# Kernel tuning notes

Hardware: AMD Instinct MI355X
Metric: run time of the kernel (lower is better)

## Reference

```python
import jax, jax.numpy as jnp
import numpy as np

H = 256
W = 256
RADIUS = 1.5
TAU = 1.0
EPS = 1e-8


def _ndc_grid(h, w):
    ys, xs = jnp.meshgrid(jnp.arange(h, dtype=jnp.float32), jnp.arange(w, dtype=jnp.float32), indexing='ij')
    xs = xs / (w - 1) * 2.0 - 1.0
    ys = ys / (h - 1) * 2.0 - 1.0
    return jnp.stack([xs.ravel(), ys.ravel()], 0)  # [2, N]


def _make_rt(key, b, v):
    # near-identity extrinsics: identity rotation + small random translation
    t = jax.random.normal(key, (b, v, 3), dtype=jnp.float32) * 0.05
    rt = jnp.tile(jnp.eye(4, dtype=jnp.float32), (b, v, 1, 1))
    rt = rt.at[:, :, :3, 3].set(t)
    return rt


def setup_inputs() -> dict:
    key = jax.random.key(0)
    ks = jax.random.split(key, 4)
    B, V, C = 2, 3, 32
    depths = jax.random.uniform(ks[0], (B, V, 1, H, W), jnp.float32, 1.0, 3.0)
    feats = jax.random.normal(ks[1], (B, V, C, H, W), jnp.float32)
    K = jnp.tile(jnp.eye(4, dtype=jnp.float32), (B, 1, 1))
    K = K.at[:, 0, 0].set(1.2).at[:, 1, 1].set(1.2)  # NDC-space focal lengths
    src_RTs = _make_rt(ks[2], B, V)
    src_RTinvs = jnp.linalg.inv(src_RTs)
    dst_RTs = _make_rt(ks[3], B, 1)
    dst_RTinvs = jnp.linalg.inv(dst_RTs)
    return {"depths": depths, "feats": feats, "K": K, "src_RTs": src_RTs,
            "src_RTinvs": src_RTinvs, "dst_RTs": dst_RTs, "dst_RTinvs": dst_RTinvs}


def _view_to_world(depth, K_inv, RTinv):
    # depth: [BV, 1, N] -> world homogeneous coords [BV, 4, N]
    grid = _ndc_grid(H, W)                                      # [2, N]
    xy = grid[None] * depth                                     # [BV, 2, N]
    pc = jnp.concatenate([xy, depth, jnp.ones_like(depth)], 1)  # [BV, 4, N]
    cam = jnp.einsum('bij,bjn->bin', K_inv, pc)
    return jnp.einsum('bij,bjn->bin', RTinv, cam)


def _world_to_view(wrld, K, RT):
    cam = jnp.einsum('bij,bjn->bin', RT, wrld)
    proj = jnp.einsum('bij,bjn->bin', K, cam)
    z = proj[:, 2:3]
    xy = proj[:, 0:2] / (z + EPS)
    xy = jnp.where(z <= 0.0, -10.0, xy)       # invalid points pushed off-screen
    return jnp.concatenate([xy, z], 1)        # [BV, 3, N]


def _splatter(pc, feats, radius):
    # pc: [BV, N, 3] (x_ndc, y_ndc, depth); feats: [BV, C, N]
    BV, N, _ = pc.shape
    C = feats.shape[1]
    x, y, z = pc[..., 0], pc[..., 1], pc[..., 2]
    px = (x + 1.0) * 0.5 * (W - 1)
    py = (y + 1.0) * 0.5 * (H - 1)
    offs = jnp.array([[dy, dx] for dy in (-1, 0, 1) for dx in (-1, 0, 1)], dtype=jnp.float32)
    ix = jnp.round(px)[..., None] + offs[:, 1]     # [BV, N, 9]
    iy = jnp.round(py)[..., None] + offs[:, 0]
    dist = jnp.sqrt((ix - px[..., None]) ** 2 + (iy - py[..., None]) ** 2 + EPS)
    w_r = jnp.maximum(0.0, 1.0 - dist / radius)    # radius-based falloff
    valid = (ix >= 0) & (ix < W) & (iy >= 0) & (iy < H) & (z[..., None] > 0)
    w_d = jnp.exp(-TAU * z)[..., None]             # depth-aware (soft z-buffer) weight
    w = w_r * w_d * valid.astype(w_r.dtype)        # [BV, N, 9]
    idx = iy.astype(jnp.int32).clip(0, H - 1) * W + ix.astype(jnp.int32).clip(0, W - 1)
    flat = (jnp.arange(BV, dtype=jnp.int32)[:, None, None] * (H * W) + idx).reshape(-1)
    w_sum = jax.ops.segment_sum(w.reshape(-1), flat, num_segments=BV * H * W)
    fw = (feats[:, :, :, None] * w[:, None, :, :]).transpose(0, 2, 3, 1).reshape(-1, C)
    f_sum = jax.ops.segment_sum(fw, flat, num_segments=BV * H * W)
    z_sum = jax.ops.segment_sum((z[..., None] * w).reshape(-1), flat, num_segments=BV * H * W)
    out_f = (f_sum / (w_sum[:, None] + EPS)).reshape(BV, H, W, C).transpose(0, 3, 1, 2)
    out_d = (z_sum / (w_sum + EPS)).reshape(BV, 1, H, W)
    return out_f, out_d


def reference(depths, feats, K, src_RTs, src_RTinvs, dst_RTs, dst_RTinvs):
    B, V, C = feats.shape[0], feats.shape[1], feats.shape[2]
    N = H * W
    d = depths.reshape(B * V, 1, N)
    f = feats.reshape(B * V, C, N)
    K_bv = jnp.repeat(K, V, axis=0)
    K_inv_bv = jnp.repeat(jnp.linalg.inv(K), V, axis=0)
    src_rtinv = src_RTinvs.reshape(B * V, 4, 4)
    dst_rt = jnp.repeat(dst_RTs[:, 0], V, axis=0)
    wrld = _view_to_world(d, K_inv_bv, src_rtinv)      # view -> world per source view
    sampler = _world_to_view(wrld, K_bv, dst_rt)       # world -> target view [BV,3,N]
    pc = sampler.transpose(0, 2, 1)                    # [BV, N, 3]
    prj_f, prj_d = _splatter(pc, f, RADIUS)
    return prj_f.reshape(B, V, C, H, W), prj_d.reshape(B, V, 1, H, W)
```

## Files before the change

kernel.cpp:

```cpp
#include <hip/hip_runtime.h>
#include <hip/hip_fp16.h>
#include <math.h>

#define H 256
#define W 256
#define HW (H * W)
#define B 2
#define V 3
#define BV (B * V)
#define C 32
#define RADIUS 1.5f
#define TAU 1.0f
#define EPS 1e-8f

#define NPIX (BV * HW)
#define NBLK (NPIX / 256)

#define GW 258
#define GH 258
#define NCELL (BV * GH * GW)
#define NSUMS ((NCELL + 255) / 256)
#define ECAP 384

__device__ __forceinline__ int swizzle_block(int bid) {
    return (bid & 7) * (NBLK / 8) + (bid >> 3);
}

__global__ void setup_kernel(const float* __restrict__ Kmat,
                             const float* __restrict__ srcRTinv,
                             const float* __restrict__ dstRT,
                             float* __restrict__ Mbuf) {
    int bv = threadIdx.x;
    if (bv >= BV) return;
    int b = bv / V;

    float a[4][8];
    for (int i = 0; i < 4; i++)
        for (int j = 0; j < 4; j++) {
            a[i][j] = Kmat[b * 16 + i * 4 + j];
            a[i][4 + j] = (i == j) ? 1.0f : 0.0f;
        }
    for (int col = 0; col < 4; col++) {
        int piv = col;
        float best = fabsf(a[col][col]);
        for (int r = col + 1; r < 4; r++) {
            float v = fabsf(a[r][col]);
            if (v > best) { best = v; piv = r; }
        }
        if (piv != col) {
            for (int j = 0; j < 8; j++) {
                float t = a[col][j]; a[col][j] = a[piv][j]; a[piv][j] = t;
            }
        }
        float s = 1.0f / a[col][col];
        for (int j = 0; j < 8; j++) a[col][j] *= s;
        for (int r = 0; r < 4; r++) {
            if (r == col) continue;
            float m = a[r][col];
            for (int j = 0; j < 8; j++) a[r][j] -= m * a[col][j];
        }
    }
    float Kinv[16];
    for (int i = 0; i < 4; i++)
        for (int j = 0; j < 4; j++) Kinv[i * 4 + j] = a[i][4 + j];

    float T1[16];
    const float* S = srcRTinv + bv * 16;
    for (int i = 0; i < 4; i++)
        for (int j = 0; j < 4; j++) {
            float acc = 0.0f;
            for (int k = 0; k < 4; k++) acc += S[i * 4 + k] * Kinv[k * 4 + j];
            T1[i * 4 + j] = acc;
        }
    float T2[16];
    const float* D = dstRT + b * 16;
    for (int i = 0; i < 4; i++)
        for (int j = 0; j < 4; j++) {
            float acc = 0.0f;
            for (int k = 0; k < 4; k++) acc += D[i * 4 + k] * T1[k * 4 + j];
            T2[i * 4 + j] = acc;
        }
    const float* Kb = Kmat + b * 16;
    for (int i = 0; i < 4; i++)
        for (int j = 0; j < 4; j++) {
            float acc = 0.0f;
            for (int k = 0; k < 4; k++) acc += Kb[i * 4 + k] * T2[k * 4 + j];
            Mbuf[bv * 16 + i * 4 + j] = acc;
        }
}

__global__ __launch_bounds__(256) void project_count_kernel(
    const float* __restrict__ depths, const float* __restrict__ Mbuf,
    float4* __restrict__ staging, int2* __restrict__ meta) {
    int gid = swizzle_block(blockIdx.x) * 256 + threadIdx.x;
    int bv = gid >> 16;
    int n = gid & (HW - 1);

    float xn = (float)(n & (W - 1)) * (2.0f / (W - 1)) - 1.0f;
    float yn = (float)(n >> 8)      * (2.0f / (H - 1)) - 1.0f;
    float d = depths[gid];
    const float* M = Mbuf + bv * 16;
    float X = xn * d, Y = yn * d;
    float p0 = M[0] * X + M[1] * Y + M[2] * d + M[3];
    float p1 = M[4] * X + M[5] * Y + M[6] * d + M[7];
    float z  = M[8] * X + M[9] * Y + M[10] * d + M[11];

    int cell = -1;
    float px = 0.0f, py = 0.0f;
    if (z > 0.0f) {
        float inv = 1.0f / (z + EPS);
        px = (p0 * inv + 1.0f) * 0.5f * (float)(W - 1);
        py = (p1 * inv + 1.0f) * 0.5f * (float)(H - 1);
        float rx = rintf(px), ry = rintf(py);
        if (rx >= -1.0f && rx <= (float)W && ry >= -1.0f && ry <= (float)H) {
            cell = bv * (GH * GW) + ((int)ry + 1) * GW + ((int)rx + 1);
            atomicAdd(&meta[cell].y, 1);
        }
    }
    staging[gid] = make_float4(px, py, z, __int_as_float(cell));
}

__global__ __launch_bounds__(256) void alloc1_kernel(int2* __restrict__ meta,
                                                     int* __restrict__ bsum) {
    int i = blockIdx.x * 256 + threadIdx.x;
    int c = (i < NCELL) ? meta[i].y : 0;
    int lane = threadIdx.x & 63;
    int wid = threadIdx.x >> 6;
    int x = c;
#pragma unroll
    for (int dlt = 1; dlt < 64; dlt <<= 1) {
        int y = __shfl_up(x, dlt);
        if (lane >= dlt) x += y;
    }
    __shared__ int wsum[4];
    __shared__ int wbase[4];
    if (lane == 63) wsum[wid] = x;
    __syncthreads();
    if (threadIdx.x == 0) {
        int s0 = wsum[0], s1 = wsum[1], s2 = wsum[2], s3 = wsum[3];
        wbase[0] = 0; wbase[1] = s0; wbase[2] = s0 + s1; wbase[3] = s0 + s1 + s2;
        bsum[blockIdx.x] = s0 + s1 + s2 + s3;
    }
    __syncthreads();
    if (i <= NCELL) meta[i].x = wbase[wid] + (x - c);
}

__global__ __launch_bounds__(256) void alloc2_kernel(int* __restrict__ bsum) {
    __shared__ int wsum[4];
    __shared__ int wbase[4];
    __shared__ int carry_s;
    int tid = threadIdx.x;
    int lane = tid & 63;
    int wid = tid >> 6;
    if (tid == 0) carry_s = 0;
    __syncthreads();
    const int nchunk = (NSUMS + 255) / 256;
    for (int ch = 0; ch < nchunk; ch++) {
        int i = ch * 256 + tid;
        int c = (i < NSUMS) ? bsum[i] : 0;
        int x = c;
#pragma unroll
        for (int dlt = 1; dlt < 64; dlt <<= 1) {
            int y = __shfl_up(x, dlt);
            if (lane >= dlt) x += y;
        }
        if (lane == 63) wsum[wid] = x;
        __syncthreads();
        if (tid == 0) {
            int cr = carry_s;
            int s0 = wsum[0], s1 = wsum[1], s2 = wsum[2], s3 = wsum[3];
            wbase[0] = cr; wbase[1] = cr + s0; wbase[2] = cr + s0 + s1;
            wbase[3] = cr + s0 + s1 + s2;
            carry_s = cr + s0 + s1 + s2 + s3;
        }
        __syncthreads();
        if (i < NSUMS) bsum[i] = wbase[wid] + (x - c);
        __syncthreads();
    }
}

__global__ __launch_bounds__(256) void fill_kernel(
    const float* __restrict__ feats, const float4* __restrict__ staging,
    const int* __restrict__ bsum, int2* __restrict__ meta,
    float4* __restrict__ entries16, uint4* __restrict__ entriesF) {
    __shared__ float sm[C][257];
    int blk = blockIdx.x;
    int bv = blk >> 8;
    int n0 = (blk & 255) << 8;
    int tid = threadIdx.x;
    const float* src = feats + (size_t)bv * C * HW + n0;
#pragma unroll
    for (int c = 0; c < C; c++) sm[c][tid] = src[(size_t)c * HW + tid];
    __syncthreads();

    int gid = (bv << 16) | (n0 + tid);
    float4 s = staging[gid];
    int cell = __float_as_int(s.w);
    if (cell < 0) return;
    int pos = bsum[cell >> 8] + atomicAdd(&meta[cell].x, 1);

    float wd = expf(-TAU * s.z);
    entries16[pos] = make_float4(s.x, s.y, s.z, wd);

    uint4* dst = entriesF + (size_t)pos * 4;
#pragma unroll
    for (int g = 0; g < 4; g++) {
        __half2 h0 = __floats2half2_rn(sm[g * 8 + 0][tid], sm[g * 8 + 1][tid]);
        __half2 h1 = __floats2half2_rn(sm[g * 8 + 2][tid], sm[g * 8 + 3][tid]);
        __half2 h2 = __floats2half2_rn(sm[g * 8 + 4][tid], sm[g * 8 + 5][tid]);
        __half2 h3 = __floats2half2_rn(sm[g * 8 + 6][tid], sm[g * 8 + 7][tid]);
        uint4 pk;
        pk.x = *(unsigned int*)&h0;
        pk.y = *(unsigned int*)&h1;
        pk.z = *(unsigned int*)&h2;
        pk.w = *(unsigned int*)&h3;
        dst[g] = pk;
    }
}

__global__ __launch_bounds__(256) void gather_kernel(
    const float4* __restrict__ entries16, const uint4* __restrict__ entriesF,
    const int2* __restrict__ meta, const int* __restrict__ bsum,
    float* __restrict__ out) {
    __shared__ int cs_s[18][19];
    __shared__ int row_rs[18];
    __shared__ int row_off[18];
    __shared__ int row_sl[18];
    __shared__ float4 lds_e[ECAP];
    __shared__ uint4 lds_f[ECAP * 5];

    int sblk = swizzle_block(blockIdx.x);
    int bv = sblk >> 8;
    int t = sblk & 255;
    int ty0 = (t >> 4) << 4;
    int tx0 = (t & 15) << 4;
    int tid = threadIdx.x;
    int cellbase = bv * (GH * GW);

    for (int i = tid; i < 18 * 19; i += 256) {
        int hr = i / 19, lc = i - hr * 19;
        int cg = cellbase + (ty0 + hr) * GW + (tx0 + lc);
        int2 m = meta[cg];
        cs_s[hr][lc] = bsum[cg >> 8] + m.x - m.y;
    }
    __syncthreads();
    if (tid == 0) {
        int off = 0;
        for (int hr = 0; hr < 18; hr++) {
            int rs = cs_s[hr][0];
            int len = cs_s[hr][18] - rs;
            int sl = min(len, ECAP - off);
            if (sl < 0) sl = 0;
            row_rs[hr] = rs;
            row_off[hr] = off;
            row_sl[hr] = sl;
            off += sl;
        }
    }
    __syncthreads();
    {
        int wid = tid >> 6, lane = tid & 63;
        for (int hr = wid; hr < 18; hr += 4) {
            int rs = row_rs[hr], off = row_off[hr], sl = row_sl[hr];
            for (int j = lane; j < sl; j += 64)
                lds_e[off + j] = entries16[rs + j];
            int j0 = lane >> 2, g = lane & 3;
            for (int j = j0; j < sl; j += 16)
                lds_f[(off + j) * 5 + g] = entriesF[(size_t)(rs + j) * 4 + g];
        }
    }
    __syncthreads();

    int lx = tid & 15, ly = tid >> 4;
    float qx = (float)(tx0 + lx);
    float qy = (float)(ty0 + ly);

    float wsum = 0.0f, zwsum = 0.0f;
    float facc[C];
#pragma unroll
    for (int c = 0; c < C; c++) facc[c] = 0.0f;

    auto accum_lds = [&](float4 v, int li) {
        float ddx = qx - v.x, ddy = qy - v.y;
        float d2 = ddx * ddx + ddy * ddy + EPS;
        if (d2 < RADIUS * RADIUS) {
            float dist = sqrtf(d2);
            float wr = 1.0f - dist * (1.0f / RADIUS);
            float w = wr * v.w;
            wsum += w;
            zwsum += v.z * w;
#pragma unroll
            for (int g = 0; g < 4; g++) {
                uint4 fv = lds_f[li * 5 + g];
                const __half2* h2 = (const __half2*)&fv;
#pragma unroll
                for (int k = 0; k < 4; k++) {
                    float2 f2 = __half22float2(h2[k]);
                    facc[g * 8 + 2 * k]     = fmaf(w, f2.x, facc[g * 8 + 2 * k]);
                    facc[g * 8 + 2 * k + 1] = fmaf(w, f2.y, facc[g * 8 + 2 * k + 1]);
                }
            }
        }
    };
    auto accum_glb = [&](float4 v, int pos) {
        float ddx = qx - v.x, ddy = qy - v.y;
        float d2 = ddx * ddx + ddy * ddy + EPS;
        if (d2 < RADIUS * RADIUS) {
            float dist = sqrtf(d2);
            float wr = 1.0f - dist * (1.0f / RADIUS);
            float w = wr * v.w;
            wsum += w;
            zwsum += v.z * w;
            const uint4* fp = entriesF + (size_t)pos * 4;
#pragma unroll
            for (int g = 0; g < 4; g++) {
                uint4 fv = fp[g];
                const __half2* h2 = (const __half2*)&fv;
#pragma unroll
                for (int k = 0; k < 4; k++) {
                    float2 f2 = __half22float2(h2[k]);
                    facc[g * 8 + 2 * k]     = fmaf(w, f2.x, facc[g * 8 + 2 * k]);
                    facc[g * 8 + 2 * k + 1] = fmaf(w, f2.y, facc[g * 8 + 2 * k + 1]);
                }
            }
        }
    };

#pragma unroll
    for (int dy = 0; dy < 3; dy++) {
        int hr = ly + dy;
        int s = cs_s[hr][lx];
        int e = cs_s[hr][lx + 3];
        int rs = row_rs[hr];
        int off = row_off[hr];
        int sEnd = rs + row_sl[hr];
        int e1 = min(e, sEnd);
        for (int pos = s; pos < e1; ++pos) {
            int li = off + (pos - rs);
            accum_lds(lds_e[li], li);
        }
        for (int pos = max(s, sEnd); pos < e; ++pos)
            accum_glb(entries16[pos], pos);
    }

    int q = ((ty0 + ly) << 8) | (tx0 + lx);
    int gid = (bv << 16) | q;
    float invw = 1.0f / (wsum + EPS);
    float* ob = out + (size_t)bv * C * HW + q;
#pragma unroll
    for (int c = 0; c < C; c++) ob[(size_t)c * HW] = facc[c] * invw;
    out[(size_t)BV * C * HW + gid] = zwsum * invw;
}

extern "C" void kernel_launch(void* const* d_in, const int* in_sizes, int n_in,
                              void* d_out, int out_size, void* d_ws, size_t ws_size,
                              hipStream_t stream) {
    const float* depths   = (const float*)d_in[0];
    const float* feats    = (const float*)d_in[1];
    const float* Kmat     = (const float*)d_in[2];
    const float* srcRTinv = (const float*)d_in[4];
    const float* dstRT    = (const float*)d_in[5];
    float* out = (float*)d_out;

    char* ws = (char*)d_ws;
    size_t off_entriesF = 0;
    size_t off_entries16 = off_entriesF + (size_t)NPIX * 64;
    size_t off_staging = off_entries16 + (size_t)NPIX * 16;
    size_t off_meta = off_staging + (size_t)NPIX * 16;
    size_t off_bsum = off_meta + (size_t)(NCELL + 1) * 8;
    size_t off_M = off_bsum + (size_t)NSUMS * 4 + 16;
    size_t needed = off_M + (size_t)BV * 16 * 4;

    if (ws_size < needed) {
        hipMemsetAsync(d_out, 0, (size_t)out_size * 4, stream);
        return;
    }

    uint4* entriesF   = (uint4*)(ws + off_entriesF);
    float4* entries16 = (float4*)(ws + off_entries16);
    float4* staging   = (float4*)(ws + off_staging);
    int2* meta        = (int2*)(ws + off_meta);
    int* bsum         = (int*)(ws + off_bsum);
    float* Mbuf       = (float*)(ws + off_M);

    hipMemsetAsync(meta, 0, (size_t)(NCELL + 1) * 8, stream);
    setup_kernel<<<1, 64, 0, stream>>>(Kmat, srcRTinv, dstRT, Mbuf);
    project_count_kernel<<<NBLK, 256, 0, stream>>>(depths, Mbuf, staging, meta);
    alloc1_kernel<<<NSUMS, 256, 0, stream>>>(meta, bsum);
    alloc2_kernel<<<1, 256, 0, stream>>>(bsum);
    fill_kernel<<<NBLK, 256, 0, stream>>>(feats, staging, bsum, meta,
                                          entries16, entriesF);
    gather_kernel<<<NBLK, 256, 0, stream>>>(entries16, entriesF, meta, bsum,
                                            out);
}
```

Before: 183.6 us.

## Fuse projection with feature transpose and bin by 16-bit indices

Moves the 4x4 matrix setup into the projection kernel, which now also converts features to half precision and writes them in source-pixel order. The fill kernel becomes a light index-fill pass that stores only a 16-bit pixel index per cell slot instead of scattering 80-byte records. The gather kernel then reads projection and feature records indirectly through these indices, and its row-offset prefix scan now uses a warp shuffle instead of a serial loop. This removes the large scattered write of feature records. In exchange the gather reads become indirect and less coalesced, and the LDS staging capacity is slightly reduced.

New measurement: 190.9 us. 3.9% more time.

```diff
diff --git a/kernel.cpp b/kernel.cpp
--- a/kernel.cpp
+++ b/kernel.cpp
@@ -20,20 +20,17 @@
 #define GH 258
 #define NCELL (BV * GH * GW)
 #define NSUMS ((NCELL + 255) / 256)
-#define ECAP 384
+#define ECAP 368
 
 __device__ __forceinline__ int swizzle_block(int bid) {
     return (bid & 7) * (NBLK / 8) + (bid >> 3);
 }
 
-__global__ void setup_kernel(const float* __restrict__ Kmat,
-                             const float* __restrict__ srcRTinv,
-                             const float* __restrict__ dstRT,
-                             float* __restrict__ Mbuf) {
-    int bv = threadIdx.x;
-    if (bv >= BV) return;
+__device__ void compute_M(int bv, const float* __restrict__ Kmat,
+                          const float* __restrict__ srcRTinv,
+                          const float* __restrict__ dstRT,
+                          float* __restrict__ Mout) {
     int b = bv / V;
-
     float a[4][8];
     for (int i = 0; i < 4; i++)
         for (int j = 0; j < 4; j++) {
@@ -85,25 +82,37 @@
         for (int j = 0; j < 4; j++) {
             float acc = 0.0f;
             for (int k = 0; k < 4; k++) acc += Kb[i * 4 + k] * T2[k * 4 + j];
-            Mbuf[bv * 16 + i * 4 + j] = acc;
-        }
-}
-
-__global__ __launch_bounds__(256) void project_count_kernel(
-    const float* __restrict__ depths, const float* __restrict__ Mbuf,
-    float4* __restrict__ staging, int2* __restrict__ meta) {
-    int gid = swizzle_block(blockIdx.x) * 256 + threadIdx.x;
-    int bv = gid >> 16;
-    int n = gid & (HW - 1);
-
+            Mout[i * 4 + j] = acc;
+        }
+}
+
+__global__ __launch_bounds__(256) void project_kernel(
+    const float* __restrict__ depths, const float* __restrict__ feats,
+    const float* __restrict__ Kmat, const float* __restrict__ srcRTinv,
+    const float* __restrict__ dstRT, float4* __restrict__ proj4,
+    int* __restrict__ cellArr, int2* __restrict__ meta,
+    uint4* __restrict__ featsT) {
+    __shared__ float sm[C][257];
+    __shared__ float Msh[16];
+    int blk = swizzle_block(blockIdx.x);
+    int bv = blk >> 8;
+    int n0 = (blk & 255) << 8;
+    int tid = threadIdx.x;
+    if (tid == 0) compute_M(bv, Kmat, srcRTinv, dstRT, Msh);
+    const float* src = feats + (size_t)bv * C * HW + n0;
+#pragma unroll
+    for (int c = 0; c < C; c++) sm[c][tid] = src[(size_t)c * HW + tid];
+    __syncthreads();
+
+    int n = n0 + tid;
+    int gid = (bv << 16) | n;
     float xn = (float)(n & (W - 1)) * (2.0f / (W - 1)) - 1.0f;
     float yn = (float)(n >> 8)      * (2.0f / (H - 1)) - 1.0f;
     float d = depths[gid];
-    const float* M = Mbuf + bv * 16;
     float X = xn * d, Y = yn * d;
-    float p0 = M[0] * X + M[1] * Y + M[2] * d + M[3];
-    float p1 = M[4] * X + M[5] * Y + M[6] * d + M[7];
-    float z  = M[8] * X + M[9] * Y + M[10] * d + M[11];
+    float p0 = Msh[0] * X + Msh[1] * Y + Msh[2]  * d + Msh[3];
+    float p1 = Msh[4] * X + Msh[5] * Y + Msh[6]  * d + Msh[7];
+    float z  = Msh[8] * X + Msh[9] * Y + Msh[10] * d + Msh[11];
 
     int cell = -1;
     float px = 0.0f, py = 0.0f;
@@ -117,92 +126,11 @@
             atomicAdd(&meta[cell].y, 1);
         }
     }
-    staging[gid] = make_float4(px, py, z, __int_as_float(cell));
-}
-
-__global__ __launch_bounds__(256) void alloc1_kernel(int2* __restrict__ meta,
-                                                     int* __restrict__ bsum) {
-    int i = blockIdx.x * 256 + threadIdx.x;
-    int c = (i < NCELL) ? meta[i].y : 0;
-    int lane = threadIdx.x & 63;
-    int wid = threadIdx.x >> 6;
-    int x = c;
-#pragma unroll
-    for (int dlt = 1; dlt < 64; dlt <<= 1) {
-        int y = __shfl_up(x, dlt);
-        if (lane >= dlt) x += y;
-    }
-    __shared__ int wsum[4];
-    __shared__ int wbase[4];
-    if (lane == 63) wsum[wid] = x;
-    __syncthreads();
-    if (threadIdx.x == 0) {
-        int s0 = wsum[0], s1 = wsum[1], s2 = wsum[2], s3 = wsum[3];
-        wbase[0] = 0; wbase[1] = s0; wbase[2] = s0 + s1; wbase[3] = s0 + s1 + s2;
-        bsum[blockIdx.x] = s0 + s1 + s2 + s3;
-    }
-    __syncthreads();
-    if (i <= NCELL) meta[i].x = wbase[wid] + (x - c);
-}
-
-__global__ __launch_bounds__(256) void alloc2_kernel(int* __restrict__ bsum) {
-    __shared__ int wsum[4];
-    __shared__ int wbase[4];
-    __shared__ int carry_s;
-    int tid = threadIdx.x;
-    int lane = tid & 63;
-    int wid = tid >> 6;
-    if (tid == 0) carry_s = 0;
-    __syncthreads();
-    const int nchunk = (NSUMS + 255) / 256;
-    for (int ch = 0; ch < nchunk; ch++) {
-        int i = ch * 256 + tid;
-        int c = (i < NSUMS) ? bsum[i] : 0;
-        int x = c;
-#pragma unroll
-        for (int dlt = 1; dlt < 64; dlt <<= 1) {
-            int y = __shfl_up(x, dlt);
-            if (lane >= dlt) x += y;
-        }
-        if (lane == 63) wsum[wid] = x;
-        __syncthreads();
-        if (tid == 0) {
-            int cr = carry_s;
-            int s0 = wsum[0], s1 = wsum[1], s2 = wsum[2], s3 = wsum[3];
-            wbase[0] = cr; wbase[1] = cr + s0; wbase[2] = cr + s0 + s1;
-            wbase[3] = cr + s0 + s1 + s2;
-            carry_s = cr + s0 + s1 + s2 + s3;
-        }
-        __syncthreads();
-        if (i < NSUMS) bsum[i] = wbase[wid] + (x - c);
-        __syncthreads();
-    }
-}
-
-__global__ __launch_bounds__(256) void fill_kernel(
-    const float* __restrict__ feats, const float4* __restrict__ staging,
-    const int* __restrict__ bsum, int2* __restrict__ meta,
-    float4* __restrict__ entries16, uint4* __restrict__ entriesF) {
-    __shared__ float sm[C][257];
-    int blk = blockIdx.x;
-    int bv = blk >> 8;
-    int n0 = (blk & 255) << 8;
-    int tid = threadIdx.x;
-    const float* src = feats + (size_t)bv * C * HW + n0;
-#pragma unroll
-    for (int c = 0; c < C; c++) sm[c][tid] = src[(size_t)c * HW + tid];
-    __syncthreads();
-
-    int gid = (bv << 16) | (n0 + tid);
-    float4 s = staging[gid];
-    int cell = __float_as_int(s.w);
-    if (cell < 0) return;
-    int pos = bsum[cell >> 8] + atomicAdd(&meta[cell].x, 1);
-
-    float wd = expf(-TAU * s.z);
-    entries16[pos] = make_float4(s.x, s.y, s.z, wd);
-
-    uint4* dst = entriesF + (size_t)pos * 4;
+    float wd = (z > -80.0f) ? expf(-TAU * z) : 0.0f;
+    proj4[gid] = make_float4(px, py, z, wd);
+    cellArr[gid] = cell;
+
+    uint4* dst = featsT + (size_t)gid * 4;
 #pragma unroll
     for (int g = 0; g < 4; g++) {
         __half2 h0 = __floats2half2_rn(sm[g * 8 + 0][tid], sm[g * 8 + 1][tid]);
@@ -218,16 +146,84 @@
     }
 }
 
+__global__ __launch_bounds__(256) void alloc1_kernel(int2* __restrict__ meta,
+                                                     int* __restrict__ bsum) {
+    int i = blockIdx.x * 256 + threadIdx.x;
+    int c = (i < NCELL) ? meta[i].y : 0;
+    int lane = threadIdx.x & 63;
+    int wid = threadIdx.x >> 6;
+    int x = c;
+#pragma unroll
+    for (int dlt = 1; dlt < 64; dlt <<= 1) {
+        int y = __shfl_up(x, dlt);
+        if (lane >= dlt) x += y;
+    }
+    __shared__ int wsum[4];
+    __shared__ int wbase[4];
+    if (lane == 63) wsum[wid] = x;
+    __syncthreads();
+    if (threadIdx.x == 0) {
+        int s0 = wsum[0], s1 = wsum[1], s2 = wsum[2], s3 = wsum[3];
+        wbase[0] = 0; wbase[1] = s0; wbase[2] = s0 + s1; wbase[3] = s0 + s1 + s2;
+        bsum[blockIdx.x] = s0 + s1 + s2 + s3;
+    }
+    __syncthreads();
+    if (i <= NCELL) meta[i].x = wbase[wid] + (x - c);
+}
+
+__global__ __launch_bounds__(256) void alloc2_kernel(int* __restrict__ bsum) {
+    __shared__ int wsum[4];
+    __shared__ int wbase[4];
+    __shared__ int carry_s;
+    int tid = threadIdx.x;
+    int lane = tid & 63;
+    int wid = tid >> 6;
+    if (tid == 0) carry_s = 0;
+    __syncthreads();
+    const int nchunk = (NSUMS + 255) / 256;
+    for (int ch = 0; ch < nchunk; ch++) {
+        int i = ch * 256 + tid;
+        int c = (i < NSUMS) ? bsum[i] : 0;
+        int x = c;
+#pragma unroll
+        for (int dlt = 1; dlt < 64; dlt <<= 1) {
+            int y = __shfl_up(x, dlt);
+            if (lane >= dlt) x += y;
+        }
+        if (lane == 63) wsum[wid] = x;
+        __syncthreads();
+        if (tid == 0) {
+            int cr = carry_s;
+            int s0 = wsum[0], s1 = wsum[1], s2 = wsum[2], s3 = wsum[3];
+            wbase[0] = cr; wbase[1] = cr + s0; wbase[2] = cr + s0 + s1;
+            wbase[3] = cr + s0 + s1 + s2;
+            carry_s = cr + s0 + s1 + s2 + s3;
+        }
+        __syncthreads();
+        if (i < NSUMS) bsum[i] = wbase[wid] + (x - c);
+        __syncthreads();
+    }
+}
+
+__global__ __launch_bounds__(256) void idx_fill_kernel(
+    const int* __restrict__ cellArr, const int* __restrict__ bsum,
+    int2* __restrict__ meta, unsigned short* __restrict__ idx_g) {
+    int gid = blockIdx.x * 256 + threadIdx.x;
+    int cell = cellArr[gid];
+    if (cell < 0) return;
+    int pos = bsum[cell >> 8] + atomicAdd(&meta[cell].x, 1);
+    idx_g[pos] = (unsigned short)(gid & (HW - 1));
+}
+
 __global__ __launch_bounds__(256) void gather_kernel(
-    const float4* __restrict__ entries16, const uint4* __restrict__ entriesF,
-    const int2* __restrict__ meta, const int* __restrict__ bsum,
-    float* __restrict__ out) {
+    const float4* __restrict__ proj4, const float4* __restrict__ featsT,
+    const unsigned short* __restrict__ idx_g, const int2* __restrict__ meta,
+    const int* __restrict__ bsum, float* __restrict__ out) {
     __shared__ int cs_s[18][19];
     __shared__ int row_rs[18];
     __shared__ int row_off[18];
     __shared__ int row_sl[18];
-    __shared__ float4 lds_e[ECAP];
-    __shared__ uint4 lds_f[ECAP * 5];
+    __shared__ float4 lds_rec[ECAP * 5];
 
     int sblk = swizzle_block(blockIdx.x);
     int bv = sblk >> 8;
@@ -236,6 +232,7 @@
     int tx0 = (t & 15) << 4;
     int tid = threadIdx.x;
     int cellbase = bv * (GH * GW);
+    int pbase = bv << 16;
 
     for (int i = tid; i < 18 * 19; i += 256) {
         int hr = i / 19, lc = i - hr * 19;
@@ -244,17 +241,24 @@
         cs_s[hr][lc] = bsum[cg >> 8] + m.x - m.y;
     }
     __syncthreads();
-    if (tid == 0) {
-        int off = 0;
-        for (int hr = 0; hr < 18; hr++) {
-            int rs = cs_s[hr][0];
-            int len = cs_s[hr][18] - rs;
-            int sl = min(len, ECAP - off);
+    if (tid < 32) {
+        int l = tid;
+        int start = 0, len = 0;
+        if (l < 18) { start = cs_s[l][0]; len = cs_s[l][18] - start; }
+        int x = len;
+#pragma unroll
+        for (int dlt = 1; dlt < 32; dlt <<= 1) {
+            int y = __shfl_up(x, dlt);
+            if (l >= dlt) x += y;
+        }
+        if (l < 18) {
+            int off = x - len;
+            row_rs[l] = start;
+            row_off[l] = off;
+            int sl = ECAP - off;
+            sl = min(sl, len);
             if (sl < 0) sl = 0;
-            row_rs[hr] = rs;
-            row_off[hr] = off;
-            row_sl[hr] = sl;
-            off += sl;
+            row_sl[l] = sl;
         }
     }
     __syncthreads();
@@ -262,11 +266,15 @@
         int wid = tid >> 6, lane = tid & 63;
         for (int hr = wid; hr < 18; hr += 4) {
             int rs = row_rs[hr], off = row_off[hr], sl = row_sl[hr];
-            for (int j = lane; j < sl; j += 64)
-                lds_e[off + j] = entries16[rs + j];
+            for (int j = lane; j < sl; j += 64) {
+                int n = idx_g[rs + j];
+                lds_rec[(off + j) * 5] = proj4[pbase + n];
+            }
             int j0 = lane >> 2, g = lane & 3;
-            for (int j = j0; j < sl; j += 16)
-                lds_f[(off + j) * 5 + g] = entriesF[(size_t)(rs + j) * 4 + g];
+            for (int j = j0; j < sl; j += 16) {
+                int n = idx_g[rs + j];
+                lds_rec[(off + j) * 5 + 1 + g] = featsT[(size_t)(pbase + n) * 4 + g];
+            }
         }
     }
     __syncthreads();
@@ -280,7 +288,8 @@
 #pragma unroll
     for (int c = 0; c < C; c++) facc[c] = 0.0f;
 
-    auto accum_lds = [&](float4 v, int li) {
+    auto accum_lds = [&](int li) {
+        float4 v = lds_rec[li * 5];
         float ddx = qx - v.x, ddy = qy - v.y;
         float d2 = ddx * ddx + ddy * ddy + EPS;
         if (d2 < RADIUS * RADIUS) {
@@ -291,8 +300,8 @@
             zwsum += v.z * w;
 #pragma unroll
             for (int g = 0; g < 4; g++) {
-                uint4 fv = lds_f[li * 5 + g];
-                const __half2* h2 = (const __half2*)&fv;
+                float4 fvf = lds_rec[li * 5 + 1 + g];
+                const __half2* h2 = (const __half2*)&fvf;
 #pragma unroll
                 for (int k = 0; k < 4; k++) {
                     float2 f2 = __half22float2(h2[k]);
@@ -302,7 +311,9 @@
             }
         }
     };
-    auto accum_glb = [&](float4 v, int pos) {
+    auto accum_glb = [&](int pos) {
+        int n = idx_g[pos];
+        float4 v = proj4[pbase + n];
         float ddx = qx - v.x, ddy = qy - v.y;
         float d2 = ddx * ddx + ddy * ddy + EPS;
         if (d2 < RADIUS * RADIUS) {
@@ -311,11 +322,11 @@
             float w = wr * v.w;
             wsum += w;
             zwsum += v.z * w;
-            const uint4* fp = entriesF + (size_t)pos * 4;
+            const float4* fp = featsT + (size_t)(pbase + n) * 4;
 #pragma unroll
             for (int g = 0; g < 4; g++) {
-                uint4 fv = fp[g];
-                const __half2* h2 = (const __half2*)&fv;
+                float4 fvf = fp[g];
+                const __half2* h2 = (const __half2*)&fvf;
 #pragma unroll
                 for (int k = 0; k < 4; k++) {
                     float2 f2 = __half22float2(h2[k]);
@@ -335,16 +346,14 @@
         int off = row_off[hr];
         int sEnd = rs + row_sl[hr];
         int e1 = min(e, sEnd);
-        for (int pos = s; pos < e1; ++pos) {
-            int li = off + (pos - rs);
-            accum_lds(lds_e[li], li);
-        }
+        for (int pos = s; pos < e1; ++pos)
+            accum_lds(off + (pos - rs));
         for (int pos = max(s, sEnd); pos < e; ++pos)
-            accum_glb(entries16[pos], pos);
+            accum_glb(pos);
     }
 
     int q = ((ty0 + ly) << 8) | (tx0 + lx);
-    int gid = (bv << 16) | q;
+    int gid = pbase | q;
     float invw = 1.0f / (wsum + EPS);
     float* ob = out + (size_t)bv * C * HW + q;
 #pragma unroll
@@ -363,33 +372,33 @@
     float* out = (float*)d_out;
 
     char* ws = (char*)d_ws;
-    size_t off_entriesF = 0;
-    size_t off_entries16 = off_entriesF + (size_t)NPIX * 64;
-    size_t off_staging = off_entries16 + (size_t)NPIX * 16;
-    size_t off_meta = off_staging + (size_t)NPIX * 16;
-    size_t off_bsum = off_meta + (size_t)(NCELL + 1) * 8;
-    size_t off_M = off_bsum + (size_t)NSUMS * 4 + 16;
-    size_t needed = off_M + (size_t)BV * 16 * 4;
+    size_t off_featsT = 0;
+    size_t off_proj = off_featsT + (size_t)NPIX * 64;
+    size_t off_cell = off_proj + (size_t)NPIX * 16;
+    size_t off_meta = off_cell + (size_t)NPIX * 4;
+    size_t off_idx = off_meta + (size_t)(NCELL + 1) * 8;
+    size_t off_bsum = off_idx + (size_t)NPIX * 2;
+    size_t needed = off_bsum + (size_t)NSUMS * 4 + 16;
 
     if (ws_size < needed) {
         hipMemsetAsync(d_out, 0, (size_t)out_size * 4, stream);
         return;
     }
 
-    uint4* entriesF   = (uint4*)(ws + off_entriesF);
-    float4* entries16 = (float4*)(ws + off_entries16);
-    float4* staging   = (float4*)(ws + off_staging);
-    int2* meta        = (int2*)(ws + off_meta);
-    int* bsum         = (int*)(ws + off_bsum);
-    float* Mbuf       = (float*)(ws + off_M);
+    uint4* featsT       = (uint4*)(ws + off_featsT);
+    float4* proj4       = (float4*)(ws + off_proj);
+    int* cellArr        = (int*)(ws + off_cell);
+    int2* meta          = (int2*)(ws + off_meta);
+    unsigned short* idx = (unsigned short*)(ws + off_idx);
+    int* bsum           = (int*)(ws + off_bsum);
 
     hipMemsetAsync(meta, 0, (size_t)(NCELL + 1) * 8, stream);
-    setup_kernel<<<1, 64, 0, stream>>>(Kmat, srcRTinv, dstRT, Mbuf);
-    project_count_kernel<<<NBLK, 256, 0, stream>>>(depths, Mbuf, staging, meta);
+    project_kernel<<<NBLK, 256, 0, stream>>>(depths, feats, Kmat, srcRTinv,
+                                             dstRT, proj4, cellArr, meta,
+                                             featsT);
     alloc1_kernel<<<NSUMS, 256, 0, stream>>>(meta, bsum);
     alloc2_kernel<<<1, 256, 0, stream>>>(bsum);
-    fill_kernel<<<NBLK, 256, 0, stream>>>(feats, staging, bsum, meta,
-                                          entries16, entriesF);
-    gather_kernel<<<NBLK, 256, 0, stream>>>(entries16, entriesF, meta, bsum,
-                                            out);
-}
+    idx_fill_kernel<<<NBLK, 256, 0, stream>>>(cellArr, bsum, meta, idx);
+    gather_kernel<<<NBLK, 256, 0, stream>>>(proj4, (const float4*)featsT, idx,
+                                            meta, bsum, out);
+}
```
